# Optimization experiments

Hardware: AMD Instinct MI355X
Metric: run time of the kernel (lower is better)

Reference implementation:

```python
import jax, jax.numpy as jnp
import numpy as np

B = 8                                   # point clouds per batch
NS = [65536, 16384, 4096, 1024, 256]    # points per scale (stride-4 downsampling)
CS = [32, 64, 128, 256, 512]            # encoder channels per scale
K = 3
BN_EPS = 1e-5


def setup_inputs() -> dict:
    key = jax.random.key(0)
    ks = iter(jax.random.split(key, 64))
    inp = {}
    for i, (n, c) in enumerate(zip(NS, CS)):
        inp[f"p{i}"] = jax.random.uniform(next(ks), (n, 3), jnp.float32)
        inp[f"f{i}"] = jax.random.normal(next(ks), (n, c), jnp.float32)
        inp[f"b{i}"] = jnp.repeat(jnp.arange(B, dtype=jnp.int32), n // B)
    # FP stage mlps: a:(4->3) [768,256,256], b:(3->2) [384,128,128],
    #               c:(2->1) [192,64,64],   d:(1->0) [96,32,32]
    cfg = {"a": (CS[3] + CS[4], CS[3]), "b": (CS[2] + CS[3], CS[2]),
           "c": (CS[1] + CS[2], CS[1]), "d": (CS[0] + CS[1], CS[0])}
    for s, (cin, ch) in cfg.items():
        for j, ci in ((1, cin), (2, ch)):
            inp[f"w{s}{j}"] = jax.random.normal(next(ks), (ci, ch), jnp.float32) / float(np.sqrt(ci))
            inp[f"bias{s}{j}"] = jnp.zeros((ch,), jnp.float32)
            inp[f"g{s}{j}"] = jnp.ones((ch,), jnp.float32)
            inp[f"bt{s}{j}"] = jnp.zeros((ch,), jnp.float32)
    return inp


def _knn_interpolate(x2, p2, p1):
    """torch_geometric.nn.knn_interpolate with k=3; equal-sized sorted batches."""
    n1, n2, c = p1.shape[0] // B, p2.shape[0] // B, x2.shape[1]
    p1b, p2b = p1.reshape(B, n1, 3), p2.reshape(B, n2, 3)
    x2b = x2.reshape(B, n2, c)
    # squared dists via |a|^2 + |b|^2 - 2ab (avoids [B,n1,n2,3] temporary)
    d2 = (jnp.sum(p1b * p1b, -1)[:, :, None] + jnp.sum(p2b * p2b, -1)[:, None, :]
          - 2.0 * jnp.einsum('bnd,bmd->bnm', p1b, p2b))
    neg_d2, idx = jax.lax.top_k(-d2, K)              # [B, n1, K]
    w = 1.0 / jnp.maximum(-neg_d2, 1e-16)            # inverse squared distance
    gath = jax.vmap(lambda x, i: x[i])(x2b, idx)     # [B, n1, K, c]
    out = jnp.einsum('bnk,bnkc->bnc', w, gath) / jnp.sum(w, -1, keepdims=True)
    return out.reshape(B * n1, c)


def _lin_bn_relu(x, w, bias, gamma, beta):
    h = x @ w + bias
    mu = jnp.mean(h, 0)
    var = jnp.mean((h - mu) ** 2, 0)
    return jax.nn.relu((h - mu) * jax.lax.rsqrt(var + BN_EPS) * gamma + beta)


def _fp_stage(p_fine, f_fine, p_coarse, f_coarse, w1, b1, g1, bt1, w2, b2, g2, bt2):
    up = _knn_interpolate(f_coarse, p_coarse, p_fine)
    x = jnp.concatenate([f_fine, up], axis=1)
    x = _lin_bn_relu(x, w1, b1, g1, bt1)
    return _lin_bn_relu(x, w2, b2, g2, bt2)


def reference(p0, p1, p2, p3, p4, f0, f1, f2, f3, f4, b0, b1, b2, b3, b4,
              wa1, biasa1, ga1, bta1, wa2, biasa2, ga2, bta2,
              wb1, biasb1, gb1, btb1, wb2, biasb2, gb2, btb2,
              wc1, biasc1, gc1, btc1, wc2, biasc2, gc2, btc2,
              wd1, biasd1, gd1, btd1, wd2, biasd2, gd2, btd2):
    f3 = _fp_stage(p3, f3, p4, f4, wa1, biasa1, ga1, bta1, wa2, biasa2, ga2, bta2)
    f2 = _fp_stage(p2, f2, p3, f3, wb1, biasb1, gb1, btb1, wb2, biasb2, gb2, btb2)
    f1 = _fp_stage(p1, f1, p2, f2, wc1, biasc1, gc1, btc1, wc2, biasc2, gc2, btc2)
    f0 = _fp_stage(p0, f0, p1, f1, wd1, biasd1, gd1, btd1, wd2, biasd2, gd2, btd2)
    return f0
```

## Files before the change

### kernel.cpp

```cpp
#include <hip/hip_runtime.h>

#define BN_EPS 1e-5f

typedef unsigned short us;

__device__ __forceinline__ float bf2f(us u) {
    union { unsigned int i; float f; } v; v.i = ((unsigned int)u) << 16; return v.f;
}
__device__ __forceinline__ us f2bf(float f) {
    unsigned int x = __float_as_uint(f);
    x += 0x7fffu + ((x >> 16) & 1u);
    return (us)(x >> 16);
}
__device__ __forceinline__ float ldf(const void* p, size_t i, int f32) {
    return f32 ? ((const float*)p)[i] : bf2f(((const us*)p)[i]);
}

__global__ void detect_kernel(const unsigned int* __restrict__ g, int* __restrict__ flag) {
    if (threadIdx.x == 0 && blockIdx.x == 0)
        *flag = ((g[0] & 0xFFFFu) == 0u) ? 1 : 0;
}

__global__ __launch_bounds__(256)
void prep_aos_kernel(const void* __restrict__ p, float4* __restrict__ aos,
                     const int* __restrict__ pf32, int n)
{
    const int i = blockIdx.x * 256 + threadIdx.x;
    if (i >= n) return;
    const int f32 = *pf32;
    const float x = ldf(p, (size_t)3 * i + 0, f32);
    const float y = ldf(p, (size_t)3 * i + 1, f32);
    const float z = ldf(p, (size_t)3 * i + 2, f32);
    const float s2 = __fadd_rn(__fadd_rn(__fmul_rn(x, x), __fmul_rn(y, y)), __fmul_rn(z, z));
    aos[i] = make_float4(__fadd_rn(x, x), __fadd_rn(y, y), __fadd_rn(z, z), s2);
}

__device__ __forceinline__ void lexmerge33(
    const float a0, const int A0, const float a1, const int A1, const float a2, const int A2,
    const float b0, const int B0, const float b1, const int B1, const float b2, const int B2,
    float& m0, int& M0, float& m1, int& M1, float& m2, int& M2)
{
    const bool c1 = (a0 < b0) || (a0 == b0 && A0 < B0);
    m0 = c1 ? a0 : b0;  M0 = c1 ? A0 : B0;
    const float hAd = c1 ? a1 : a0;  const int hAi = c1 ? A1 : A0;
    const float hBd = c1 ? b0 : b1;  const int hBi = c1 ? B0 : B1;
    const bool c2 = (hAd < hBd) || (hAd == hBd && hAi < hBi);
    m1 = c2 ? hAd : hBd;  M1 = c2 ? hAi : hBi;
    const float gAd = c2 ? (c1 ? a2 : a1) : hAd;  const int gAi = c2 ? (c1 ? A2 : A1) : hAi;
    const float gBd = c2 ? hBd : (c1 ? b1 : b2);  const int gBi = c2 ? hBi : (c1 ? B1 : B2);
    const bool c3 = (gAd < gBd) || (gAd == gBd && gAi < gBi);
    m2 = c3 ? gAd : gBd;  M2 = c3 ? gAi : gBi;
}

template<int MODE, int SPLIT, int LEN>
__global__ __launch_bounds__(64 * SPLIT, 8)
void knn_up_kernel(
    const void* __restrict__ p_fine,
    const float4* __restrict__ aos,
    const void* __restrict__ f_coarse,
    const float* __restrict__ stats,
    const void* __restrict__ gamma,
    const void* __restrict__ beta,
    float inv_n2,
    float* __restrict__ up_out,
    const int* __restrict__ pf32,
    int n2pb, int c2)
{
    __shared__ float mrg_d[SPLIT * 64 * 3];
    __shared__ int   mrg_i[SPLIT * 64 * 3];
    __shared__ float aff_a[256], aff_b[256];
    __shared__ int   s_idx[64][3];
    __shared__ float s_w[64][3];

    const int f32 = *pf32;
    const int tid = threadIdx.x;
    const int lane = tid & 63;
    const int wv = tid >> 6;
    const int cbase = blockIdx.y * n2pb;
    const int row0 = (blockIdx.y * gridDim.x + blockIdx.x) * 64;

    if (MODE == 1) {
        for (int c = tid; c < c2; c += 64 * SPLIT) {
            float mu  = stats[c] * inv_n2;
            float var = stats[c2 + c] * inv_n2 - mu * mu;
            float a = ldf(gamma, c, f32) * rsqrtf(var + BN_EPS);
            aff_a[c] = a;
            aff_b[c] = ldf(beta, c, f32) - mu * a;
        }
    }

    {
        const int row = row0 + lane;
        const size_t b = (size_t)row * 3;
        const float px = ldf(p_fine, b + 0, f32);
        const float py = ldf(p_fine, b + 1, f32);
        const float pz = ldf(p_fine, b + 2, f32);
        const float s1 = __fadd_rn(__fadd_rn(__fmul_rn(px, px), __fmul_rn(py, py)),
                                   __fmul_rn(pz, pz));
        const int jb = wv * LEN;
        const float4* __restrict__ sl = aos + cbase + jb;
        float t0 = 1e30f, t1 = 1e30f, t2 = 1e30f;
        int i0 = jb, i1 = jb, i2 = jb;

#define KNN_UPD(CQ, JJ) {                                                     \
        const float dot2 = fmaf(pz, (CQ).z, fmaf(py, (CQ).y,                  \
                                __fmul_rn(px, (CQ).x)));                      \
        const float d = __fsub_rn(__fadd_rn(s1, (CQ).w), dot2);               \
        const int jj = (JJ);                                                  \
        const bool a0 = d < t0, a1 = d < t1, a2 = d < t2;                     \
        t2 = a1 ? t1 : (a2 ? d : t2);  i2 = a1 ? i1 : (a2 ? jj : i2);         \
        t1 = a0 ? t0 : (a1 ? d : t1);  i1 = a0 ? i0 : (a1 ? jj : i1);         \
        t0 = a0 ? d  : t0;             i0 = a0 ? jj : i0; }

        float4 ca = sl[0], cb = sl[1], cc = sl[2], cd = sl[3];
        for (int t = 0; t < LEN; t += 4) {
            float4 na, nb, nc, nd;
            const bool more = (t + 4) < LEN;
            if (more) { na = sl[t + 4]; nb = sl[t + 5]; nc = sl[t + 6]; nd = sl[t + 7]; }
            KNN_UPD(ca, jb + t + 0);
            KNN_UPD(cb, jb + t + 1);
            KNN_UPD(cc, jb + t + 2);
            KNN_UPD(cd, jb + t + 3);
            if (more) { ca = na; cb = nb; cc = nc; cd = nd; }
        }
#undef KNN_UPD

        const int mb = (wv * 64 + lane) * 3;
        mrg_d[mb + 0] = t0;  mrg_i[mb + 0] = cbase + i0;
        mrg_d[mb + 1] = t1;  mrg_i[mb + 1] = cbase + i1;
        mrg_d[mb + 2] = t2;  mrg_i[mb + 2] = cbase + i2;
    }
    __syncthreads();

    if (tid < 64) {
        float d0 = mrg_d[tid * 3 + 0], d1 = mrg_d[tid * 3 + 1], d2 = mrg_d[tid * 3 + 2];
        int   j0 = mrg_i[tid * 3 + 0], j1 = mrg_i[tid * 3 + 1], j2 = mrg_i[tid * 3 + 2];
        #pragma unroll
        for (int w = 1; w < SPLIT; ++w) {
            const int mb = (w * 64 + tid) * 3;
            const float e0 = mrg_d[mb + 0], e1 = mrg_d[mb + 1], e2 = mrg_d[mb + 2];
            const int   k0 = mrg_i[mb + 0], k1 = mrg_i[mb + 1], k2 = mrg_i[mb + 2];
            float n0, n1, n2v; int ni0, ni1, ni2;
            lexmerge33(d0, j0, d1, j1, d2, j2,
                       e0, k0, e1, k1, e2, k2,
                       n0, ni0, n1, ni1, n2v, ni2);
            d0 = n0; j0 = ni0; d1 = n1; j1 = ni1; d2 = n2v; j2 = ni2;
        }
        s_idx[tid][0] = j0;  s_w[tid][0] = __fdiv_rn(1.0f, fmaxf(d0, 1e-16f));
        s_idx[tid][1] = j1;  s_w[tid][1] = __fdiv_rn(1.0f, fmaxf(d1, 1e-16f));
        s_idx[tid][2] = j2;  s_w[tid][2] = __fdiv_rn(1.0f, fmaxf(d2, 1e-16f));
    }
    __syncthreads();

    for (int p = wv; p < 64; p += SPLIT) {
        const int row = row0 + p;
        const int g0 = s_idx[p][0], g1 = s_idx[p][1], g2 = s_idx[p][2];
        const float w0 = s_w[p][0], w1 = s_w[p][1], w2 = s_w[p][2];
        const float den = __fadd_rn(__fadd_rn(w0, w1), w2);
        float* __restrict__ urow = up_out + (size_t)row * c2;
        for (int c = lane; c < c2; c += 64) {
            float v0, v1, v2;
            if (MODE == 0) {
                v0 = ldf(f_coarse, (size_t)g0 * c2 + c, f32);
                v1 = ldf(f_coarse, (size_t)g1 * c2 + c, f32);
                v2 = ldf(f_coarse, (size_t)g2 * c2 + c, f32);
            } else {
                const float* fc = (const float*)f_coarse;
                const float aa = aff_a[c], bb = aff_b[c];
                v0 = fmaxf(aa * fc[(size_t)g0 * c2 + c] + bb, 0.f);
                v1 = fmaxf(aa * fc[(size_t)g1 * c2 + c] + bb, 0.f);
                v2 = fmaxf(aa * fc[(size_t)g2 * c2 + c] + bb, 0.f);
            }
            const float num = fmaf(w2, v2, fmaf(w1, v1, __fmul_rn(w0, v0)));
            urow[c] = __fdiv_rn(num, den);
        }
    }
}

__global__ __launch_bounds__(256)
void gemm1_bn_kernel(const void* __restrict__ Ffine,
                     const float* __restrict__ Up,
                     const void* __restrict__ W,
                     const void* __restrict__ bias,
                     float* __restrict__ H,
                     float* __restrict__ stats_out,
                     const int* __restrict__ pf32,
                     int M, int c1, int c2, int N)
{
    __shared__ __align__(16) float As[16][68];
    __shared__ __align__(16) float Bs[16][68];
    __shared__ float s_sum[64], s_sq[64];

    const int f32 = *pf32;
    const int K = c1 + c2;
    const int tid = threadIdx.x;
    const int tx = tid & 15, ty = tid >> 4;
    const int n0 = blockIdx.x * 64, m0 = blockIdx.y * 64;

    if (tid < 64) { s_sum[tid] = 0.f; s_sq[tid] = 0.f; }

    const int a_m = tid >> 2;
    const int a_k = (tid & 3) << 2;
    const int b_k = tid >> 4;
    const int b_n = (tid & 15) << 2;
    const int row = m0 + a_m;

    float avp[4]; float4 bvp;
    {
        const int k = a_k;
        if (k < c1) {
            if (f32) {
                const float4 v = *(const float4*)((const float*)Ffine + (size_t)row * c1 + k);
                avp[0] = v.x; avp[1] = v.y; avp[2] = v.z; avp[3] = v.w;
            } else {
                const ushort4 u = *(const ushort4*)((const us*)Ffine + (size_t)row * c1 + k);
                avp[0] = bf2f(u.x); avp[1] = bf2f(u.y); avp[2] = bf2f(u.z); avp[3] = bf2f(u.w);
            }
        } else {
            const float4 v = *(const float4*)(Up + (size_t)row * c2 + (k - c1));
            avp[0] = v.x; avp[1] = v.y; avp[2] = v.z; avp[3] = v.w;
        }
        bvp = make_float4(0.f, 0.f, 0.f, 0.f);
        if (n0 + b_n < N) {
            const size_t wi = (size_t)b_k * N + (n0 + b_n);
            if (f32) bvp = *(const float4*)((const float*)W + wi);
            else {
                const ushort4 u = *(const ushort4*)((const us*)W + wi);
                bvp = make_float4(bf2f(u.x), bf2f(u.y), bf2f(u.z), bf2f(u.w));
            }
        }
    }

    float acc[4][4] = {};

    for (int k0 = 0; k0 < K; k0 += 16) {
        #pragma unroll
        for (int i = 0; i < 4; ++i) As[a_k + i][a_m] = avp[i];
        *(float4*)&Bs[b_k][b_n] = bvp;
        __syncthreads();

        float avn[4]; float4 bvn;
        const int kn = k0 + 16;
        if (kn < K) {
            const int k = kn + a_k;
            if (k < c1) {
                if (f32) {
                    const float4 v = *(const float4*)((const float*)Ffine + (size_t)row * c1 + k);
                    avn[0] = v.x; avn[1] = v.y; avn[2] = v.z; avn[3] = v.w;
                } else {
                    const ushort4 u = *(const ushort4*)((const us*)Ffine + (size_t)row * c1 + k);
                    avn[0] = bf2f(u.x); avn[1] = bf2f(u.y); avn[2] = bf2f(u.z); avn[3] = bf2f(u.w);
                }
            } else {
                const float4 v = *(const float4*)(Up + (size_t)row * c2 + (k - c1));
                avn[0] = v.x; avn[1] = v.y; avn[2] = v.z; avn[3] = v.w;
            }
            bvn = make_float4(0.f, 0.f, 0.f, 0.f);
            if (n0 + b_n < N) {
                const size_t wi = (size_t)(kn + b_k) * N + (n0 + b_n);
                if (f32) bvn = *(const float4*)((const float*)W + wi);
                else {
                    const ushort4 u = *(const ushort4*)((const us*)W + wi);
                    bvn = make_float4(bf2f(u.x), bf2f(u.y), bf2f(u.z), bf2f(u.w));
                }
            }
        }

        #pragma unroll
        for (int kk = 0; kk < 16; ++kk) {
            const float4 a4 = *(const float4*)&As[kk][ty << 2];
            const float4 b4 = *(const float4*)&Bs[kk][tx << 2];
            const float aarr[4] = {a4.x, a4.y, a4.z, a4.w};
            const float barr[4] = {b4.x, b4.y, b4.z, b4.w};
            #pragma unroll
            for (int i = 0; i < 4; ++i)
                #pragma unroll
                for (int j = 0; j < 4; ++j)
                    acc[i][j] = fmaf(aarr[i], barr[j], acc[i][j]);
        }
        __syncthreads();

        if (kn < K) {
            #pragma unroll
            for (int i = 0; i < 4; ++i) avp[i] = avn[i];
            bvp = bvn;
        }
    }

    float bvals[4];
    const bool colsok = (n0 + (tx << 2)) < N;
    #pragma unroll
    for (int j = 0; j < 4; ++j) {
        const int n = n0 + (tx << 2) + j;
        bvals[j] = (n < N) ? ldf(bias, n, f32) : 0.f;
    }
    float ps[4] = {0.f, 0.f, 0.f, 0.f}, pq[4] = {0.f, 0.f, 0.f, 0.f};
    #pragma unroll
    for (int i = 0; i < 4; ++i) {
        float4 hv;
        float* hvp = (float*)&hv;
        #pragma unroll
        for (int j = 0; j < 4; ++j) {
            const float v = acc[i][j] + bvals[j];
            hvp[j] = v;
            ps[j] += v;
            pq[j] = fmaf(v, v, pq[j]);
        }
        if (colsok)
            *(float4*)(H + (size_t)(m0 + (ty << 2) + i) * N + n0 + (tx << 2)) = hv;
    }
    #pragma unroll
    for (int j = 0; j < 4; ++j) {
        atomicAdd(&s_sum[(tx << 2) + j], ps[j]);
        atomicAdd(&s_sq[(tx << 2) + j], pq[j]);
    }
    __syncthreads();
    if (tid < 64) {
        const int n = n0 + tid;
        if (n < N) {
            atomicAdd(&stats_out[n], s_sum[tid]);
            atomicAdd(&stats_out[N + n], s_sq[tid]);
        }
    }
}

__global__ __launch_bounds__(256)
void gemm2_bn_kernel(const float* __restrict__ A,
                     const void* __restrict__ W,
                     const void* __restrict__ bias,
                     const float* __restrict__ stats_in,
                     const void* __restrict__ g_in,
                     const void* __restrict__ bt_in,
                     float inv_m,
                     float* __restrict__ H,
                     float* __restrict__ stats_out,
                     const int* __restrict__ pf32,
                     int M, int K, int N)
{
    __shared__ __align__(16) float As[16][68];
    __shared__ __align__(16) float Bs[16][68];
    __shared__ float aff_a[256], aff_b[256];
    __shared__ float s_sum[64], s_sq[64];

    const int f32 = *pf32;
    const int tid = threadIdx.x;
    const int tx = tid & 15, ty = tid >> 4;
    const int n0 = blockIdx.x * 64, m0 = blockIdx.y * 64;

    for (int c = tid; c < K; c += 256) {
        float mu  = stats_in[c] * inv_m;
        float var = stats_in[K + c] * inv_m - mu * mu;
        float a = ldf(g_in, c, f32) * rsqrtf(var + BN_EPS);
        aff_a[c] = a; aff_b[c] = ldf(bt_in, c, f32) - mu * a;
    }
    if (tid < 64) { s_sum[tid] = 0.f; s_sq[tid] = 0.f; }
    __syncthreads();

    const int a_m = tid >> 2;
    const int a_k = (tid & 3) << 2;
    const int b_k = tid >> 4;
    const int b_n = (tid & 15) << 2;
    const int row = m0 + a_m;

    float avp[4]; float4 bvp;
    {
        const float4 af = *(const float4*)(A + (size_t)row * K + a_k);
        avp[0] = af.x; avp[1] = af.y; avp[2] = af.z; avp[3] = af.w;
        bvp = make_float4(0.f, 0.f, 0.f, 0.f);
        if (n0 + b_n < N) {
            const size_t wi = (size_t)b_k * N + (n0 + b_n);
            if (f32) bvp = *(const float4*)((const float*)W + wi);
            else {
                const ushort4 u = *(const ushort4*)((const us*)W + wi);
                bvp = make_float4(bf2f(u.x), bf2f(u.y), bf2f(u.z), bf2f(u.w));
            }
        }
    }

    float acc[4][4] = {};

    for (int k0 = 0; k0 < K; k0 += 16) {
        #pragma unroll
        for (int i = 0; i < 4; ++i)
            As[a_k + i][a_m] = fmaxf(fmaf(aff_a[k0 + a_k + i], avp[i], aff_b[k0 + a_k + i]), 0.f);
        *(float4*)&Bs[b_k][b_n] = bvp;
        __syncthreads();

        float avn[4]; float4 bvn;
        const int kn = k0 + 16;
        if (kn < K) {
            const float4 af = *(const float4*)(A + (size_t)row * K + (kn + a_k));
            avn[0] = af.x; avn[1] = af.y; avn[2] = af.z; avn[3] = af.w;
            bvn = make_float4(0.f, 0.f, 0.f, 0.f);
            if (n0 + b_n < N) {
                const size_t wi = (size_t)(kn + b_k) * N + (n0 + b_n);
                if (f32) bvn = *(const float4*)((const float*)W + wi);
                else {
                    const ushort4 u = *(const ushort4*)((const us*)W + wi);
                    bvn = make_float4(bf2f(u.x), bf2f(u.y), bf2f(u.z), bf2f(u.w));
                }
            }
        }

        #pragma unroll
        for (int kk = 0; kk < 16; ++kk) {
            const float4 a4 = *(const float4*)&As[kk][ty << 2];
            const float4 b4 = *(const float4*)&Bs[kk][tx << 2];
            const float aarr[4] = {a4.x, a4.y, a4.z, a4.w};
            const float barr[4] = {b4.x, b4.y, b4.z, b4.w};
            #pragma unroll
            for (int i = 0; i < 4; ++i)
                #pragma unroll
                for (int j = 0; j < 4; ++j)
                    acc[i][j] = fmaf(aarr[i], barr[j], acc[i][j]);
        }
        __syncthreads();

        if (kn < K) {
            #pragma unroll
            for (int i = 0; i < 4; ++i) avp[i] = avn[i];
            bvp = bvn;
        }
    }

    float bvals[4];
    const bool colsok = (n0 + (tx << 2)) < N;
    #pragma unroll
    for (int j = 0; j < 4; ++j) {
        const int n = n0 + (tx << 2) + j;
        bvals[j] = (n < N) ? ldf(bias, n, f32) : 0.f;
    }
    float ps[4] = {0.f, 0.f, 0.f, 0.f}, pq[4] = {0.f, 0.f, 0.f, 0.f};
    #pragma unroll
    for (int i = 0; i < 4; ++i) {
        float4 hv;
        float* hvp = (float*)&hv;
        #pragma unroll
        for (int j = 0; j < 4; ++j) {
            const float v = acc[i][j] + bvals[j];
            hvp[j] = v;
            ps[j] += v;
            pq[j] = fmaf(v, v, pq[j]);
        }
        if (colsok)
            *(float4*)(H + (size_t)(m0 + (ty << 2) + i) * N + n0 + (tx << 2)) = hv;
    }
    #pragma unroll
    for (int j = 0; j < 4; ++j) {
        atomicAdd(&s_sum[(tx << 2) + j], ps[j]);
        atomicAdd(&s_sq[(tx << 2) + j], pq[j]);
    }
    __syncthreads();
    if (tid < 64) {
        const int n = n0 + tid;
        if (n < N) {
            atomicAdd(&stats_out[n], s_sum[tid]);
            atomicAdd(&stats_out[N + n], s_sq[tid]);
        }
    }
}

__global__ __launch_bounds__(256)
void finalize_kernel(const float* __restrict__ Hf, const float* __restrict__ stats,
                     const void* __restrict__ g, const void* __restrict__ bt,
                     float inv_m, void* __restrict__ out,
                     const int* __restrict__ pf32, int total)
{
    const int idx = blockIdx.x * 256 + threadIdx.x;
    if (idx >= total) return;
    const int f32 = *pf32;
    const int c = idx & 31;
    const float mu  = stats[c] * inv_m;
    const float var = stats[32 + c] * inv_m - mu * mu;
    const float a = ldf(g, c, f32) * rsqrtf(var + BN_EPS);
    const float b = ldf(bt, c, f32) - mu * a;
    const float v = fmaxf(fmaf(a, Hf[idx], b), 0.f);
    if (f32) ((float*)out)[idx] = v;
    else     ((us*)out)[idx] = f2bf(v);
}

extern "C" void kernel_launch(void* const* d_in, const int* in_sizes, int n_in,
                              void* d_out, int out_size, void* d_ws, size_t ws_size,
                              hipStream_t stream) {
    (void)in_sizes; (void)n_in; (void)out_size; (void)ws_size;
    const void* p0 = d_in[0];
    const void* f0 = d_in[1];
    const void* p1 = d_in[3];
    const void* f1 = d_in[4];
    const void* p2 = d_in[6];
    const void* f2 = d_in[7];
    const void* p3 = d_in[9];
    const void* f3 = d_in[10];
    const void* p4 = d_in[12];
    const void* f4 = d_in[13];
    const void *W1[4], *B1[4], *G1[4], *T1[4], *W2[4], *B2[4], *G2[4], *T2[4];
    for (int s = 0; s < 4; ++s) {
        const int b = 15 + s * 8;
        W1[s] = d_in[b + 0]; B1[s] = d_in[b + 1];
        G1[s] = d_in[b + 2]; T1[s] = d_in[b + 3];
        W2[s] = d_in[b + 4]; B2[s] = d_in[b + 5];
        G2[s] = d_in[b + 6]; T2[s] = d_in[b + 7];
    }

    float* stats = (float*)d_ws;
    float* st_a1 = stats + 0;
    float* st_a2 = stats + 512;
    float* st_b1 = stats + 1024;
    float* st_b2 = stats + 1280;
    float* st_c1 = stats + 1536;
    float* st_c2 = stats + 1664;
    float* st_d1 = stats + 1792;
    float* st_d2 = stats + 1856;
    int*   flag  = (int*)(stats + 1920);
    float* U = (float*)((char*)d_ws + 8192);
    float* H = U + 4194304;
    float* h2a = H + 262144;
    float* h2b = H + 524288;
    float* h2c = H + 1048576;
    float* h2d = U;
    float4* aosbuf = (float4*)H;

    hipMemsetAsync(d_ws, 0, 1920 * sizeof(float), stream);
    detect_kernel<<<1, 64, 0, stream>>>((const unsigned int*)G1[0], flag);

    prep_aos_kernel<<<1, 256, 0, stream>>>(p4, aosbuf, flag, 256);
    knn_up_kernel<0, 8, 4><<<dim3(2, 8), 512, 0, stream>>>(
        p3, aosbuf, f4, nullptr, nullptr, nullptr, 0.f, U, flag, 32, 512);
    gemm1_bn_kernel<<<dim3(4, 16), 256, 0, stream>>>(
        f3, U, W1[0], B1[0], H, st_a1, flag, 1024, 256, 512, 256);
    gemm2_bn_kernel<<<dim3(4, 16), 256, 0, stream>>>(
        H, W2[0], B2[0], st_a1, G1[0], T1[0], 1.f / 1024.f,
        h2a, st_a2, flag, 1024, 256, 256);
    prep_aos_kernel<<<4, 256, 0, stream>>>(p3, aosbuf, flag, 1024);
    knn_up_kernel<1, 8, 16><<<dim3(8, 8), 512, 0, stream>>>(
        p2, aosbuf, h2a, st_a2, G2[0], T2[0], 1.f / 1024.f, U, flag, 128, 256);
    gemm1_bn_kernel<<<dim3(2, 64), 256, 0, stream>>>(
        f2, U, W1[1], B1[1], H, st_b1, flag, 4096, 128, 256, 128);
    gemm2_bn_kernel<<<dim3(2, 64), 256, 0, stream>>>(
        H, W2[1], B2[1], st_b1, G1[1], T1[1], 1.f / 4096.f,
        h2b, st_b2, flag, 4096, 128, 128);
    prep_aos_kernel<<<16, 256, 0, stream>>>(p2, aosbuf, flag, 4096);
    knn_up_kernel<1, 16, 32><<<dim3(32, 8), 1024, 0, stream>>>(
        p1, aosbuf, h2b, st_b2, G2[1], T2[1], 1.f / 4096.f, U, flag, 512, 128);
    gemm1_bn_kernel<<<dim3(1, 256), 256, 0, stream>>>(
        f1, U, W1[2], B1[2], H, st_c1, flag, 16384, 64, 128, 64);
    gemm2_bn_kernel<<<dim3(1, 256), 256, 0, stream>>>(
        H, W2[2], B2[2], st_c1, G1[2], T1[2], 1.f / 16384.f,
        h2c, st_c2, flag, 16384, 64, 64);
    prep_aos_kernel<<<64, 256, 0, stream>>>(p1, aosbuf, flag, 16384);
    knn_up_kernel<1, 8, 256><<<dim3(128, 8), 512, 0, stream>>>(
        p0, aosbuf, h2c, st_c2, G2[2], T2[2], 1.f / 16384.f, U, flag, 2048, 64);
    gemm1_bn_kernel<<<dim3(1, 1024), 256, 0, stream>>>(
        f0, U, W1[3], B1[3], H, st_d1, flag, 65536, 32, 64, 32);
    gemm2_bn_kernel<<<dim3(1, 1024), 256, 0, stream>>>(
        H, W2[3], B2[3], st_d1, G1[3], T1[3], 1.f / 65536.f,
        h2d, st_d2, flag, 65536, 32, 32);
    finalize_kernel<<<(65536 * 32) / 256, 256, 0, stream>>>(
        h2d, st_d2, G2[3], T2[3], 1.f / 65536.f, d_out, flag, 65536 * 32);
}
```

Baseline: 500.5 us.

## Stage coarse points in LDS for the largest kNN upsampling stage

Adds a kNN-interpolate kernel that loads each batch's 2048 coarse points into shared memory as split SoA arrays and computes their squared norms. Each block then handles 64 fine points with 8 threads per point, each scanning a contiguous segment with float4 LDS reads, and merges the per-thread top-3 lists via shuffles. This replaces the separate prep_aos kernel and the global AoS reads for the final (d) stage, aiming to cut global traffic and one launch. The cost is heavier LDS use, about 32KB per block, which may limit occupancy, and each block now redundantly reloads the coarse points.

```diff
diff --git a/kernel.cpp b/kernel.cpp
--- a/kernel.cpp
+++ b/kernel.cpp
@@ -50,6 +50,135 @@
     const float gBd = c2 ? hBd : (c1 ? b1 : b2);  const int gBi = c2 ? hBi : (c1 ? B1 : B2);
     const bool c3 = (gAd < gBd) || (gAd == gBd && gAi < gBi);
     m2 = c3 ? gAd : gBd;  M2 = c3 ? gAi : gBi;
+}
+
+template<int MODE, int FPB, int SPLIT, int N2>
+__global__ __launch_bounds__(FPB * SPLIT)
+void knn_up_lds_kernel(
+    const void* __restrict__ p_fine,
+    const void* __restrict__ p_coarse,
+    const void* __restrict__ f_coarse,
+    const float* __restrict__ stats,
+    const void* __restrict__ gamma,
+    const void* __restrict__ beta,
+    float inv_n2,
+    float* __restrict__ up_out,
+    const int* __restrict__ pf32,
+    int n2pb, int c2)
+{
+    constexpr int LEN = N2 / SPLIT;
+    constexpr int PSTR = LEN + 4;
+    __shared__ __align__(16) float cpx[SPLIT * PSTR];
+    __shared__ __align__(16) float cpy[SPLIT * PSTR];
+    __shared__ __align__(16) float cpz[SPLIT * PSTR];
+    __shared__ __align__(16) float cs2[SPLIT * PSTR];
+    __shared__ float aff_a[256], aff_b[256];
+    __shared__ int   s_idx[FPB][3];
+    __shared__ float s_w[FPB][3];
+
+    const int f32 = *pf32;
+    const int tid = threadIdx.x;
+    const int cbase = blockIdx.y * n2pb;
+
+    for (int j = tid; j < N2; j += FPB * SPLIT) {
+        const size_t b = (size_t)(cbase + j) * 3;
+        const float x = ldf(p_coarse, b + 0, f32);
+        const float y = ldf(p_coarse, b + 1, f32);
+        const float z = ldf(p_coarse, b + 2, f32);
+        const int pos = (j / LEN) * PSTR + (j & (LEN - 1));
+        cpx[pos] = x; cpy[pos] = y; cpz[pos] = z;
+        cs2[pos] = __fadd_rn(__fadd_rn(__fmul_rn(x, x), __fmul_rn(y, y)), __fmul_rn(z, z));
+    }
+    if (MODE == 1) {
+        for (int c = tid; c < c2; c += FPB * SPLIT) {
+            float mu  = stats[c] * inv_n2;
+            float var = stats[c2 + c] * inv_n2 - mu * mu;
+            float a = ldf(gamma, c, f32) * rsqrtf(var + BN_EPS);
+            aff_a[c] = a;
+            aff_b[c] = ldf(beta, c, f32) - mu * a;
+        }
+    }
+    __syncthreads();
+
+    {
+        const int f = tid / SPLIT;
+        const int s = tid & (SPLIT - 1);
+        const int row = (blockIdx.y * gridDim.x + blockIdx.x) * FPB + f;
+        const size_t b = (size_t)row * 3;
+        const float px = ldf(p_fine, b + 0, f32);
+        const float py = ldf(p_fine, b + 1, f32);
+        const float pz = ldf(p_fine, b + 2, f32);
+        const float s1 = __fadd_rn(__fadd_rn(__fmul_rn(px, px), __fmul_rn(py, py)),
+                                   __fmul_rn(pz, pz));
+        const int jb = s * LEN;
+        const int base = s * PSTR;
+        float t0 = 1e30f, t1 = 1e30f, t2 = 1e30f;
+        int i0 = jb, i1 = jb, i2 = jb;
+        for (int t = 0; t < LEN; t += 4) {
+            const float4 X = *(const float4*)&cpx[base + t];
+            const float4 Y = *(const float4*)&cpy[base + t];
+            const float4 Z = *(const float4*)&cpz[base + t];
+            const float4 S = *(const float4*)&cs2[base + t];
+            #pragma unroll
+            for (int q = 0; q < 4; ++q) {
+                const float qx = ((const float*)&X)[q];
+                const float qy = ((const float*)&Y)[q];
+                const float qz = ((const float*)&Z)[q];
+                const float s2 = ((const float*)&S)[q];
+                const float dot = fmaf(pz, qz, fmaf(py, qy, __fmul_rn(px, qx)));
+                const float d = __fsub_rn(__fadd_rn(s1, s2), __fmul_rn(2.0f, dot));
+                const int jj = jb + t + q;
+                const bool a0 = d < t0, a1 = d < t1, a2 = d < t2;
+                t2 = a1 ? t1 : (a2 ? d : t2);  i2 = a1 ? i1 : (a2 ? jj : i2);
+                t1 = a0 ? t0 : (a1 ? d : t1);  i1 = a0 ? i0 : (a1 ? jj : i1);
+                t0 = a0 ? d  : t0;             i0 = a0 ? jj : i0;
+            }
+        }
+
+        #pragma unroll
+        for (int m = 1; m < SPLIT; m <<= 1) {
+            const float o0 = __shfl_xor(t0, m, 64); const int oi0 = __shfl_xor(i0, m, 64);
+            const float o1 = __shfl_xor(t1, m, 64); const int oi1 = __shfl_xor(i1, m, 64);
+            const float o2 = __shfl_xor(t2, m, 64); const int oi2 = __shfl_xor(i2, m, 64);
+            float n0, n1, n2v; int ni0, ni1, ni2;
+            lexmerge33(t0, i0, t1, i1, t2, i2,
+                       o0, oi0, o1, oi1, o2, oi2,
+                       n0, ni0, n1, ni1, n2v, ni2);
+            t0 = n0; i0 = ni0; t1 = n1; i1 = ni1; t2 = n2v; i2 = ni2;
+        }
+        if (s == 0) {
+            s_idx[f][0] = cbase + i0;  s_w[f][0] = __fdiv_rn(1.0f, fmaxf(t0, 1e-16f));
+            s_idx[f][1] = cbase + i1;  s_w[f][1] = __fdiv_rn(1.0f, fmaxf(t1, 1e-16f));
+            s_idx[f][2] = cbase + i2;  s_w[f][2] = __fdiv_rn(1.0f, fmaxf(t2, 1e-16f));
+        }
+    }
+    __syncthreads();
+
+    const int lane = tid & 63, wv = tid >> 6;
+    const int nw = (FPB * SPLIT) / 64;
+    for (int p = wv; p < FPB; p += nw) {
+        const int row = (blockIdx.y * gridDim.x + blockIdx.x) * FPB + p;
+        const int g0 = s_idx[p][0], g1 = s_idx[p][1], g2 = s_idx[p][2];
+        const float w0 = s_w[p][0], w1 = s_w[p][1], w2 = s_w[p][2];
+        const float den = __fadd_rn(__fadd_rn(w0, w1), w2);
+        float* __restrict__ urow = up_out + (size_t)row * c2;
+        for (int c = lane; c < c2; c += 64) {
+            float v0, v1, v2;
+            if (MODE == 0) {
+                v0 = ldf(f_coarse, (size_t)g0 * c2 + c, f32);
+                v1 = ldf(f_coarse, (size_t)g1 * c2 + c, f32);
+                v2 = ldf(f_coarse, (size_t)g2 * c2 + c, f32);
+            } else {
+                const float* fc = (const float*)f_coarse;
+                const float aa = aff_a[c], bb = aff_b[c];
+                v0 = fmaxf(aa * fc[(size_t)g0 * c2 + c] + bb, 0.f);
+                v1 = fmaxf(aa * fc[(size_t)g1 * c2 + c] + bb, 0.f);
+                v2 = fmaxf(aa * fc[(size_t)g2 * c2 + c] + bb, 0.f);
+            }
+            const float num = fmaf(w2, v2, fmaf(w1, v1, __fmul_rn(w0, v0)));
+            urow[c] = __fdiv_rn(num, den);
+        }
+    }
 }
 
 template<int MODE, int SPLIT, int LEN>
@@ -547,9 +676,8 @@
     gemm2_bn_kernel<<<dim3(1, 256), 256, 0, stream>>>(
         H, W2[2], B2[2], st_c1, G1[2], T1[2], 1.f / 16384.f,
         h2c, st_c2, flag, 16384, 64, 64);
-    prep_aos_kernel<<<64, 256, 0, stream>>>(p1, aosbuf, flag, 16384);
-    knn_up_kernel<1, 8, 256><<<dim3(128, 8), 512, 0, stream>>>(
-        p0, aosbuf, h2c, st_c2, G2[2], T2[2], 1.f / 16384.f, U, flag, 2048, 64);
+    knn_up_lds_kernel<1, 64, 8, 2048><<<dim3(128, 8), 512, 0, stream>>>(
+        p0, p1, h2c, st_c2, G2[2], T2[2], 1.f / 16384.f, U, flag, 2048, 64);
     gemm1_bn_kernel<<<dim3(1, 1024), 256, 0, stream>>>(
         f0, U, W1[3], B1[3], H, st_d1, flag, 65536, 32, 64, 32);
     gemm2_bn_kernel<<<dim3(1, 1024), 256, 0, stream>>>(
```

After: 501.6 us. About the same (+0.2%).
